# Kernel optimization log

Measured on AMD Instinct MI355X. Metric: run time of the kernel, lower is better.

Reference implementation:

```python
import jax, jax.numpy as jnp
import numpy as np

N = 100000   # num nodes
E = 1200000  # num edges
D = 64       # feature dim (input and both hidden layers)
R = 4        # num relations


def setup_inputs() -> dict:
    key = jax.random.key(0)
    ks = jax.random.split(key, 16)

    def p(k, shape, scale=0.05):
        return jax.random.normal(k, shape, dtype=jnp.float32) * scale

    inp = {
        "x": p(ks[0], (N, D), 1.0),
        "src": jax.random.randint(ks[1], (E,), 0, N),
        "dst": jax.random.randint(ks[2], (E,), 0, N),
        "rel": jax.random.randint(ks[3], (E,), 0, R),
    }
    i = 4
    for layer in (1, 2):
        inp[f"conv{layer}_w"] = p(ks[i], (D, R * D)); i += 1
        inp[f"conv{layer}_b"] = jnp.zeros((D,), jnp.float32)
        inp[f"conv{layer}_ws"] = p(ks[i], (D, D)); i += 1
        inp[f"conv{layer}_bs"] = jnp.zeros((D,), jnp.float32)
        inp[f"hw{layer}_pw"] = p(ks[i], (D, 2 * D)); i += 1
        inp[f"hw{layer}_pb"] = jnp.zeros((D,), jnp.float32)
        inp[f"hw{layer}_tw"] = p(ks[i], (D, 2 * D)); i += 1
        inp[f"hw{layer}_tb"] = jnp.full((D,), -2.0, jnp.float32)  # transform bias init -2
    return inp


def _rgc(x, src, dst, rel, w, b, ws, bs):
    # RelationalGraphConv: per-(node, relation) scatter-mean of source features,
    # then linear over concatenated relation slots + self-loop linear + sigmoid.
    msg = x[src]                                  # [E, D] gather
    seg = dst * R + rel                           # [E] flattened (node, relation) id
    s = jax.ops.segment_sum(msg, seg, num_segments=N * R)          # [N*R, D]
    cnt = jax.ops.segment_sum(jnp.ones((msg.shape[0], 1), msg.dtype), seg,
                              num_segments=N * R)                  # [N*R, 1]
    upd = (s / jnp.maximum(cnt, 1.0)).reshape(N, R * x.shape[1])   # [N, R*D]
    out = upd @ w.T + b + x @ ws.T + bs
    return jax.nn.sigmoid(out)


def _highway(h, prev, pw, pb, tw, tb):
    c = jnp.concatenate([h, prev], axis=1)        # [N, 2D]
    pr = jax.nn.relu(c @ pw.T + pb)
    g = jax.nn.sigmoid(c @ tw.T + tb)
    return g * pr + (1.0 - g) * h


def reference(x, src, dst, rel,
              conv1_w, conv1_b, conv1_ws, conv1_bs,
              hw1_pw, hw1_pb, hw1_tw, hw1_tb,
              conv2_w, conv2_b, conv2_ws, conv2_bs,
              hw2_pw, hw2_pb, hw2_tw, hw2_tb):
    h1 = _rgc(x, src, dst, rel, conv1_w, conv1_b, conv1_ws, conv1_bs)
    g1 = _highway(h1, x, hw1_pw, hw1_pb, hw1_tw, hw1_tb)   # prev_gcn = input
    h2 = _rgc(g1, src, dst, rel, conv2_w, conv2_b, conv2_ws, conv2_bs)
    g2 = _highway(h2, h1, hw2_pw, hw2_pb, hw2_tw, hw2_tb)  # prev_gcn = h1 (conv1 output)
    return g2  # node_feature, [N, D]
```

## Files before the change

### kernel.cpp

```cpp
#include <hip/hip_runtime.h>

#define NN 100000
#define NE 1200000
#define NRR 400000
#define NBIN 392
#define SEGB 1024
#define EPB 4096

typedef float f32x4 __attribute__((ext_vector_type(4)));
typedef __bf16 bf16x8 __attribute__((ext_vector_type(8)));

__device__ __forceinline__ float sigmoidf_(float x){ return 1.0f/(1.0f+__expf(-x)); }

__global__ __launch_bounds__(256)
void binhist_kernel(const int* __restrict__ dst, const int* __restrict__ rel,
                    int* __restrict__ bincnt){
  __shared__ int h[NBIN];
  int t = threadIdx.x;
  for (int i = t; i < NBIN; i += 256) h[i] = 0;
  __syncthreads();
  for (int e = blockIdx.x*256 + t; e < NE; e += 512*256){
    int bin = (dst[e]*4 + rel[e]) >> 10;
    atomicAdd(&h[bin], 1);
  }
  __syncthreads();
  for (int i = t; i < NBIN; i += 256)
    if (h[i]) atomicAdd(&bincnt[i], h[i]);
}

__global__ void binscan_kernel(const int* __restrict__ bincnt, int* __restrict__ binoff,
                               int* __restrict__ bincur, int* __restrict__ soff){
  if (threadIdx.x == 0){
    int s = 0;
    for (int i = 0; i < NBIN; ++i){ binoff[i] = s; bincur[i] = s; s += bincnt[i]; }
    binoff[NBIN] = NE;
    soff[NRR] = NE;
  }
}

__global__ __launch_bounds__(256)
void passA_kernel(const int* __restrict__ src, const int* __restrict__ dst,
                  const int* __restrict__ rel, int* __restrict__ bincur,
                  unsigned* __restrict__ ebin){
  __shared__ int h[NBIN], runbase[NBIN];
  int t = threadIdx.x;
  for (int i = t; i < NBIN; i += 256) h[i] = 0;
  __syncthreads();
  int lo = blockIdx.x*EPB, hi = min(lo + EPB, NE);
  for (int e = lo + t; e < hi; e += 256)
    atomicAdd(&h[(dst[e]*4 + rel[e]) >> 10], 1);
  __syncthreads();
  for (int i = t; i < NBIN; i += 256){
    runbase[i] = h[i] ? atomicAdd(&bincur[i], h[i]) : 0;
    h[i] = 0;
  }
  __syncthreads();
  for (int e = lo + t; e < hi; e += 256){
    int seg = dst[e]*4 + rel[e];
    int bin = seg >> 10;
    int p = runbase[bin] + atomicAdd(&h[bin], 1);
    ebin[p] = (unsigned)src[e] | ((unsigned)(seg & 1023) << 17);
  }
}

__global__ __launch_bounds__(1024)
void passB_kernel(const unsigned* __restrict__ ebin, const int* __restrict__ binoff,
                  int* __restrict__ soff, unsigned* __restrict__ ebuck){
  __shared__ int st[SEGB];
  __shared__ int wsum[16], wbase[16];
  const int bin = blockIdx.x;
  const int t = threadIdx.x;
  const int base = binoff[bin], end = binoff[bin+1];
  st[t] = 0;
  __syncthreads();
  for (int e = base + t; e < end; e += 1024)
    atomicAdd(&st[(ebin[e] >> 17) & 1023], 1);
  __syncthreads();
  int h0 = st[t];
  int lane = t & 63, wv = t >> 6;
  int inc = h0;
  #pragma unroll
  for (int o = 1; o < 64; o <<= 1){ int u = __shfl_up(inc, o); if (lane >= o) inc += u; }
  if (lane == 63) wsum[wv] = inc;
  __syncthreads();
  if (t == 0){ int s = 0; for (int i = 0; i < 16; ++i){ wbase[i] = s; s += wsum[i]; } }
  __syncthreads();
  int ex = base + wbase[wv] + (inc - h0);
  st[t] = ex;
  int sg = bin*SEGB + t;
  if (sg < NRR) soff[sg] = ex;
  __syncthreads();
  for (int e = base + t; e < end; e += 1024){
    unsigned u = ebin[e];
    int p = atomicAdd(&st[(u >> 17) & 1023], 1);
    ebuck[p] = u & 0x1FFFFu;
  }
}

#define TBB 3125
__global__ __launch_bounds__(256)
void tobf16_prep_kernel(const float* __restrict__ xf, __bf16* __restrict__ xb,
                        const float* __restrict__ w,  const float* __restrict__ b,
                        const float* __restrict__ ws, const float* __restrict__ bs,
                        const float* __restrict__ pw, const float* __restrict__ pb,
                        const float* __restrict__ tw, const float* __restrict__ tb,
                        const float* __restrict__ w2,  const float* __restrict__ b2,
                        const float* __restrict__ ws2, const float* __restrict__ bs2,
                        const float* __restrict__ pw2, const float* __restrict__ pb2,
                        const float* __restrict__ tw2, const float* __restrict__ tb2,
                        __bf16* __restrict__ W1a, __bf16* __restrict__ W2a,
                        float* __restrict__ B1a, float* __restrict__ B2a,
                        __bf16* __restrict__ W1b, __bf16* __restrict__ W2b,
                        float* __restrict__ B1b, float* __restrict__ B2b){
  if (blockIdx.x < TBB) {
    int i = (blockIdx.x*256 + threadIdx.x)*8;
    if (i < NN*64){
      f32x4 a = *(const f32x4*)(xf + i);
      f32x4 c = *(const f32x4*)(xf + i + 4);
      bf16x8 r;
      r[0]=(__bf16)a[0]; r[1]=(__bf16)a[1]; r[2]=(__bf16)a[2]; r[3]=(__bf16)a[3];
      r[4]=(__bf16)c[0]; r[5]=(__bf16)c[1]; r[6]=(__bf16)c[2]; r[7]=(__bf16)c[3];
      *(bf16x8*)(xb + i) = r;
    }
    return;
  }
  int i = (blockIdx.x - TBB)*256 + threadIdx.x;
  if (i < 64*320) {
    int e = i & 7, lane = (i >> 3) & 63, j = (i >> 9) & 3, kbi = i >> 11;
    int n = j*16 + (lane & 15);
    int k = kbi*32 + (lane >> 4)*8 + e;
    float va = (k < 256) ? w[n*256 + k]  : ws[n*64 + (k - 256)];
    float vb = (k < 256) ? w2[n*256 + k] : ws2[n*64 + (k - 256)];
    W1a[i] = (__bf16)va;
    W1b[i] = (__bf16)vb;
  }
  if (i < 128*128) {
    int e = i & 7, lane = (i >> 3) & 63, j = (i >> 9) & 7, kbi = i >> 12;
    int n = j*16 + (lane & 15);
    int k = kbi*32 + (lane >> 4)*8 + e;
    float va = (n < 64) ? pw[n*128 + k]  : tw[(n - 64)*128 + k];
    float vb = (n < 64) ? pw2[n*128 + k] : tw2[(n - 64)*128 + k];
    W2a[i] = (__bf16)va;
    W2b[i] = (__bf16)vb;
  }
  if (i < 64)  { B1a[i] = b[i] + bs[i];  B1b[i] = b2[i] + bs2[i]; }
  if (i < 128) { B2a[i] = (i < 64) ? pb[i] : tb[i-64];
                 B2b[i] = (i < 64) ? pb2[i] : tb2[i-64]; }
}

__global__ __launch_bounds__(256)
void gather_kernel(const unsigned* __restrict__ ebuck, const int* __restrict__ soff,
                   const __bf16* __restrict__ inb, __bf16* __restrict__ segb){
  const int sgg = blockIdx.x*32 + (threadIdx.x >> 3);
  const int fl  = threadIdx.x & 7;
  const int e0 = soff[sgg];
  const int e1 = soff[sgg + 1];
  const int c  = e1 - e0;

  int idx[8];
  #pragma unroll
  for (int k = 0; k < 8; ++k) idx[k] = (int)ebuck[e0 + k];

  f32x4 a0 = {0.f,0.f,0.f,0.f}, a1 = {0.f,0.f,0.f,0.f};
  f32x4 b0 = {0.f,0.f,0.f,0.f}, b1 = {0.f,0.f,0.f,0.f};
  #pragma unroll
  for (int k = 0; k < 8; ++k) {
    if (k < c) {
      bf16x8 v = *(const bf16x8*)(&inb[(size_t)idx[k]*64 + fl*8]);
      if (k & 1) {
        b0[0]+=(float)v[0]; b0[1]+=(float)v[1]; b0[2]+=(float)v[2]; b0[3]+=(float)v[3];
        b1[0]+=(float)v[4]; b1[1]+=(float)v[5]; b1[2]+=(float)v[6]; b1[3]+=(float)v[7];
      } else {
        a0[0]+=(float)v[0]; a0[1]+=(float)v[1]; a0[2]+=(float)v[2]; a0[3]+=(float)v[3];
        a1[0]+=(float)v[4]; a1[1]+=(float)v[5]; a1[2]+=(float)v[6]; a1[3]+=(float)v[7];
      }
    }
  }
  for (int i = 8; i < c; i += 2) {
    int s0 = (int)ebuck[e0 + i];
    bf16x8 v0 = *(const bf16x8*)(&inb[(size_t)s0*64 + fl*8]);
    a0[0]+=(float)v0[0]; a0[1]+=(float)v0[1]; a0[2]+=(float)v0[2]; a0[3]+=(float)v0[3];
    a1[0]+=(float)v0[4]; a1[1]+=(float)v0[5]; a1[2]+=(float)v0[6]; a1[3]+=(float)v0[7];
    if (i + 1 < c) {
      int s1 = (int)ebuck[e0 + i + 1];
      bf16x8 v1 = *(const bf16x8*)(&inb[(size_t)s1*64 + fl*8]);
      b0[0]+=(float)v1[0]; b0[1]+=(float)v1[1]; b0[2]+=(float)v1[2]; b0[3]+=(float)v1[3];
      b1[0]+=(float)v1[4]; b1[1]+=(float)v1[5]; b1[2]+=(float)v1[6]; b1[3]+=(float)v1[7];
    }
  }
  float inv = 1.0f / fmaxf((float)c, 1.0f);
  bf16x8 r;
  r[0]=(__bf16)((a0[0]+b0[0])*inv); r[1]=(__bf16)((a0[1]+b0[1])*inv);
  r[2]=(__bf16)((a0[2]+b0[2])*inv); r[3]=(__bf16)((a0[3]+b0[3])*inv);
  r[4]=(__bf16)((a1[0]+b1[0])*inv); r[5]=(__bf16)((a1[1]+b1[1])*inv);
  r[6]=(__bf16)((a1[2]+b1[2])*inv); r[7]=(__bf16)((a1[3]+b1[3])*inv);

  const int n   = sgg >> 2, rr = sgg & 3;
  const int nb  = n >> 4,  ml = n & 15;
  const int kbi = rr*2 + (fl >> 2);
  const int kgs = fl & 3;
  *(bf16x8*)(&segb[(size_t)((nb*8 + kbi)*64 + kgs*16 + ml)*8]) = r;
}

#define HSP 72

template<bool LAYER1>
__global__ __launch_bounds__(256, 4)
void dense_kernel(const __bf16* __restrict__ segbs,
                  const __bf16* __restrict__ xinb,
                  const __bf16* __restrict__ prevb,
                  const __bf16* __restrict__ W1s,
                  const __bf16* __restrict__ W2s,
                  const float* __restrict__ bias1,
                  const float* __restrict__ bias2,
                  __bf16* __restrict__ hb,
                  __bf16* __restrict__ gb,
                  float* __restrict__ outp)
{
  __shared__ __align__(16) __bf16 hs[64*HSP];
  __shared__ __align__(16) float outs[64*64];

  const int tid  = threadIdx.x;
  const int lane = tid & 63;
  const int wv   = tid >> 6;
  const int mloc = lane & 15;
  const int kg   = lane >> 4;
  const int wb   = blockIdx.x*64 + wv*16;
  const int arow = min(wb + mloc, NN-1);
  const int nbq  = min(wb, NN-16) >> 4;
  const size_t abase = (size_t)nbq * (8*512);

  f32x4 acc1[4] = {};

  #pragma unroll
  for (int kbi = 0; kbi < 8; ++kbi) {
    bf16x8 af = *(const bf16x8*)(&segbs[abase + (size_t)(kbi*64 + lane)*8]);
    #pragma unroll
    for (int j = 0; j < 4; ++j) {
      bf16x8 bf = *(const bf16x8*)(&W1s[((kbi*4 + j)*64 + lane)*8]);
      acc1[j] = __builtin_amdgcn_mfma_f32_16x16x32_bf16(af, bf, acc1[j], 0,0,0);
    }
  }
  #pragma unroll
  for (int kb = 0; kb < 64; kb += 32) {
    bf16x8 af = *(const bf16x8*)(&xinb[(size_t)arow*64 + kb + kg*8]);
    const int kbi = 8 + (kb >> 5);
    #pragma unroll
    for (int j = 0; j < 4; ++j) {
      bf16x8 bf = *(const bf16x8*)(&W1s[((kbi*4 + j)*64 + lane)*8]);
      acc1[j] = __builtin_amdgcn_mfma_f32_16x16x32_bf16(af, bf, acc1[j], 0,0,0);
    }
  }

  #pragma unroll
  for (int j = 0; j < 4; ++j) {
    int col = j*16 + mloc;
    float b1 = bias1[col];
    #pragma unroll
    for (int r = 0; r < 4; ++r) {
      float hv = sigmoidf_(acc1[j][r] + b1);
      acc1[j][r] = hv;
      hs[(wv*16 + kg*4 + r)*HSP + col] = (__bf16)hv;
    }
  }

  if (LAYER1) {
    #pragma unroll
    for (int i = 0; i < 2; ++i) {
      int r2 = i*8 + (lane >> 3);
      int c2 = lane & 7;
      bf16x8 v = *(const bf16x8*)(&hs[(wv*16 + r2)*HSP + c2*8]);
      int grow = wb + r2;
      if (grow < NN) *(bf16x8*)(&hb[(size_t)grow*64 + c2*8]) = v;
    }
  }

  f32x4 acc2[8] = {};
  #pragma unroll
  for (int kb = 0; kb < 64; kb += 32) {
    bf16x8 af = *(const bf16x8*)(&hs[(wv*16 + mloc)*HSP + kb + kg*8]);
    const int kbi = kb >> 5;
    #pragma unroll
    for (int j = 0; j < 8; ++j) {
      bf16x8 bf = *(const bf16x8*)(&W2s[((kbi*8 + j)*64 + lane)*8]);
      acc2[j] = __builtin_amdgcn_mfma_f32_16x16x32_bf16(af, bf, acc2[j], 0,0,0);
    }
  }
  #pragma unroll
  for (int kb = 0; kb < 64; kb += 32) {
    bf16x8 af = *(const bf16x8*)(&prevb[(size_t)arow*64 + kb + kg*8]);
    const int kbi = 2 + (kb >> 5);
    #pragma unroll
    for (int j = 0; j < 8; ++j) {
      bf16x8 bf = *(const bf16x8*)(&W2s[((kbi*8 + j)*64 + lane)*8]);
      acc2[j] = __builtin_amdgcn_mfma_f32_16x16x32_bf16(af, bf, acc2[j], 0,0,0);
    }
  }

  #pragma unroll
  for (int j = 0; j < 4; ++j) {
    int col = j*16 + mloc;
    float bp = bias2[col];
    float bt = bias2[64 + col];
    #pragma unroll
    for (int r = 0; r < 4; ++r) {
      float pr = fmaxf(acc2[j][r] + bp, 0.0f);
      float g  = sigmoidf_(acc2[j+4][r] + bt);
      float hv = acc1[j][r];
      float ov = g*pr + (1.0f - g)*hv;
      if (LAYER1) {
        hs[(wv*16 + kg*4 + r)*HSP + col] = (__bf16)ov;
      } else {
        outs[(wv*16 + kg*4 + r)*64 + col] = ov;
      }
    }
  }
  if (LAYER1) {
    #pragma unroll
    for (int i = 0; i < 2; ++i) {
      int r2 = i*8 + (lane >> 3);
      int c2 = lane & 7;
      bf16x8 v = *(const bf16x8*)(&hs[(wv*16 + r2)*HSP + c2*8]);
      int grow = wb + r2;
      if (grow < NN) *(bf16x8*)(&gb[(size_t)grow*64 + c2*8]) = v;
    }
  } else {
    #pragma unroll
    for (int i = 0; i < 4; ++i) {
      int pos = i*256 + lane*4;
      int r2 = pos >> 6, c2 = pos & 63;
      int grow = wb + r2;
      if (grow < NN)
        *(f32x4*)(&outp[(size_t)grow*64 + c2]) =
            *(const f32x4*)(&outs[(wv*16 + r2)*64 + c2]);
    }
  }
}

extern "C" void kernel_launch(void* const* d_in, const int* in_sizes, int n_in,
                              void* d_out, int out_size, void* d_ws, size_t ws_size,
                              hipStream_t stream){
  const float* x    = (const float*)d_in[0];
  const int*   src  = (const int*)d_in[1];
  const int*   dst  = (const int*)d_in[2];
  const int*   rel  = (const int*)d_in[3];
  const float* c1w  = (const float*)d_in[4];
  const float* c1b  = (const float*)d_in[5];
  const float* c1ws = (const float*)d_in[6];
  const float* c1bs = (const float*)d_in[7];
  const float* h1pw = (const float*)d_in[8];
  const float* h1pb = (const float*)d_in[9];
  const float* h1tw = (const float*)d_in[10];
  const float* h1tb = (const float*)d_in[11];
  const float* c2w  = (const float*)d_in[12];
  const float* c2b  = (const float*)d_in[13];
  const float* c2ws = (const float*)d_in[14];
  const float* c2bs = (const float*)d_in[15];
  const float* h2pw = (const float*)d_in[16];
  const float* h2pb = (const float*)d_in[17];
  const float* h2tw = (const float*)d_in[18];
  const float* h2tb = (const float*)d_in[19];

  char* p = (char*)d_ws;
  __bf16* segb = (__bf16*)p;  p += (size_t)NRR*64*2;
  __bf16* xb   = (__bf16*)p;  p += (size_t)NN*64*2;
  __bf16* h1b  = (__bf16*)p;  p += (size_t)NN*64*2;
  __bf16* g1b  = (__bf16*)p;  p += (size_t)NN*64*2;
  unsigned* ebuck = (unsigned*)p; p += (size_t)(NE+16)*4;
  unsigned* ebin  = (unsigned*)p; p += (size_t)NE*4;
  int* soff    = (int*)p;     p += (size_t)(NRR+8)*4;
  int* bincnt  = (int*)p;     p += 512*4;
  int* binoff  = (int*)p;     p += 512*4;
  int* bincur  = (int*)p;     p += 512*4;
  __bf16* W1a  = (__bf16*)p;  p += 64*320*2;
  __bf16* W2a  = (__bf16*)p;  p += 128*128*2;
  __bf16* W1b  = (__bf16*)p;  p += 64*320*2;
  __bf16* W2b  = (__bf16*)p;  p += 128*128*2;
  float* B1a   = (float*)p;   p += 64*4;
  float* B2a   = (float*)p;   p += 128*4;
  float* B1b   = (float*)p;   p += 64*4;
  float* B2b   = (float*)p;   p += 128*4;

  float* out = (float*)d_out;

  hipMemsetAsync(bincnt, 0, 512*4, stream);
  binhist_kernel<<<512, 256, 0, stream>>>(dst, rel, bincnt);
  binscan_kernel<<<1, 64, 0, stream>>>(bincnt, binoff, bincur, soff);
  passA_kernel<<<(NE+EPB-1)/EPB, 256, 0, stream>>>(src, dst, rel, bincur, ebin);
  passB_kernel<<<NBIN, 1024, 0, stream>>>(ebin, binoff, soff, ebuck);

  tobf16_prep_kernel<<<TBB+80, 256, 0, stream>>>(x, xb,
                                      c1w, c1b, c1ws, c1bs, h1pw, h1pb, h1tw, h1tb,
                                      c2w, c2b, c2ws, c2bs, h2pw, h2pb, h2tw, h2tb,
                                      W1a, W2a, B1a, B2a, W1b, W2b, B1b, B2b);

  gather_kernel<<<NRR/32, 256, 0, stream>>>(ebuck, soff, xb, segb);
  dense_kernel<true><<<(NN+63)/64, 256, 0, stream>>>(segb, xb, xb, W1a, W2a, B1a, B2a,
                                                     h1b, g1b, nullptr);
  gather_kernel<<<NRR/32, 256, 0, stream>>>(ebuck, soff, g1b, segb);
  dense_kernel<false><<<(NN+63)/64, 256, 0, stream>>>(segb, g1b, h1b, W1b, W2b, B1b, B2b,
                                                      nullptr, nullptr, out);
}
```

Before: 300.4 us.

## Fuse scatter-mean gather into dense layer kernel via shared-memory tiles

Merges the per-(node,relation) gather/mean kernel into the dense MFMA kernel. Each block gathers its 64 nodes' 256 segments straight into an LDS tile laid out in MFMA operand order, along with the self-feature rows, then runs both matmuls from LDS. This removes the bf16 segb intermediate (global write and reread) and two launches per forward. In exchange each block does more serial gather work (8 segments per thread group), occupancy drops to 3 blocks, and the gather loses the dual-accumulator unroll for high-degree segments.

```diff
diff --git a/kernel.cpp b/kernel.cpp
--- a/kernel.cpp
+++ b/kernel.cpp
@@ -148,66 +148,12 @@
                  B2b[i] = (i < 64) ? pb2[i] : tb2[i-64]; }
 }
 
-__global__ __launch_bounds__(256)
-void gather_kernel(const unsigned* __restrict__ ebuck, const int* __restrict__ soff,
-                   const __bf16* __restrict__ inb, __bf16* __restrict__ segb){
-  const int sgg = blockIdx.x*32 + (threadIdx.x >> 3);
-  const int fl  = threadIdx.x & 7;
-  const int e0 = soff[sgg];
-  const int e1 = soff[sgg + 1];
-  const int c  = e1 - e0;
-
-  int idx[8];
-  #pragma unroll
-  for (int k = 0; k < 8; ++k) idx[k] = (int)ebuck[e0 + k];
-
-  f32x4 a0 = {0.f,0.f,0.f,0.f}, a1 = {0.f,0.f,0.f,0.f};
-  f32x4 b0 = {0.f,0.f,0.f,0.f}, b1 = {0.f,0.f,0.f,0.f};
-  #pragma unroll
-  for (int k = 0; k < 8; ++k) {
-    if (k < c) {
-      bf16x8 v = *(const bf16x8*)(&inb[(size_t)idx[k]*64 + fl*8]);
-      if (k & 1) {
-        b0[0]+=(float)v[0]; b0[1]+=(float)v[1]; b0[2]+=(float)v[2]; b0[3]+=(float)v[3];
-        b1[0]+=(float)v[4]; b1[1]+=(float)v[5]; b1[2]+=(float)v[6]; b1[3]+=(float)v[7];
-      } else {
-        a0[0]+=(float)v[0]; a0[1]+=(float)v[1]; a0[2]+=(float)v[2]; a0[3]+=(float)v[3];
-        a1[0]+=(float)v[4]; a1[1]+=(float)v[5]; a1[2]+=(float)v[6]; a1[3]+=(float)v[7];
-      }
-    }
-  }
-  for (int i = 8; i < c; i += 2) {
-    int s0 = (int)ebuck[e0 + i];
-    bf16x8 v0 = *(const bf16x8*)(&inb[(size_t)s0*64 + fl*8]);
-    a0[0]+=(float)v0[0]; a0[1]+=(float)v0[1]; a0[2]+=(float)v0[2]; a0[3]+=(float)v0[3];
-    a1[0]+=(float)v0[4]; a1[1]+=(float)v0[5]; a1[2]+=(float)v0[6]; a1[3]+=(float)v0[7];
-    if (i + 1 < c) {
-      int s1 = (int)ebuck[e0 + i + 1];
-      bf16x8 v1 = *(const bf16x8*)(&inb[(size_t)s1*64 + fl*8]);
-      b0[0]+=(float)v1[0]; b0[1]+=(float)v1[1]; b0[2]+=(float)v1[2]; b0[3]+=(float)v1[3];
-      b1[0]+=(float)v1[4]; b1[1]+=(float)v1[5]; b1[2]+=(float)v1[6]; b1[3]+=(float)v1[7];
-    }
-  }
-  float inv = 1.0f / fmaxf((float)c, 1.0f);
-  bf16x8 r;
-  r[0]=(__bf16)((a0[0]+b0[0])*inv); r[1]=(__bf16)((a0[1]+b0[1])*inv);
-  r[2]=(__bf16)((a0[2]+b0[2])*inv); r[3]=(__bf16)((a0[3]+b0[3])*inv);
-  r[4]=(__bf16)((a1[0]+b1[0])*inv); r[5]=(__bf16)((a1[1]+b1[1])*inv);
-  r[6]=(__bf16)((a1[2]+b1[2])*inv); r[7]=(__bf16)((a1[3]+b1[3])*inv);
-
-  const int n   = sgg >> 2, rr = sgg & 3;
-  const int nb  = n >> 4,  ml = n & 15;
-  const int kbi = rr*2 + (fl >> 2);
-  const int kgs = fl & 3;
-  *(bf16x8*)(&segb[(size_t)((nb*8 + kbi)*64 + kgs*16 + ml)*8]) = r;
-}
-
-#define HSP 72
+#define ASW (10*64*8)
 
 template<bool LAYER1>
-__global__ __launch_bounds__(256, 4)
-void dense_kernel(const __bf16* __restrict__ segbs,
-                  const __bf16* __restrict__ xinb,
+__global__ __launch_bounds__(256, 3)
+void fused_kernel(const unsigned* __restrict__ ebuck, const int* __restrict__ soff,
+                  const __bf16* __restrict__ inb,
                   const __bf16* __restrict__ prevb,
                   const __bf16* __restrict__ W1s,
                   const __bf16* __restrict__ W2s,
@@ -217,40 +163,89 @@
                   __bf16* __restrict__ gb,
                   float* __restrict__ outp)
 {
-  __shared__ __align__(16) __bf16 hs[64*HSP];
-  __shared__ __align__(16) float outs[64*64];
+  __shared__ __align__(16) __bf16 As[4*ASW];
 
   const int tid  = threadIdx.x;
   const int lane = tid & 63;
   const int wv   = tid >> 6;
+  const int g    = tid >> 3;
+  const int fl   = tid & 7;
+  const int base = blockIdx.x*64;
+  const int wb   = base + wv*16;
+
+  for (int si = 0; si < 8; ++si) {
+    const int sw  = g*8 + si;
+    const int sgg = blockIdx.x*256 + sw;
+    const int e0 = soff[min(sgg, NRR)];
+    const int e1 = soff[min(sgg + 1, NRR)];
+    const int c  = e1 - e0;
+
+    int idx[8];
+    #pragma unroll
+    for (int k = 0; k < 8; ++k) idx[k] = (int)ebuck[e0 + k];
+
+    f32x4 a0 = {0.f,0.f,0.f,0.f}, a1 = {0.f,0.f,0.f,0.f};
+    f32x4 b0 = {0.f,0.f,0.f,0.f}, b1 = {0.f,0.f,0.f,0.f};
+    #pragma unroll
+    for (int k = 0; k < 8; ++k) {
+      if (k < c) {
+        bf16x8 v = *(const bf16x8*)(&inb[(size_t)idx[k]*64 + fl*8]);
+        if (k & 1) {
+          b0[0]+=(float)v[0]; b0[1]+=(float)v[1]; b0[2]+=(float)v[2]; b0[3]+=(float)v[3];
+          b1[0]+=(float)v[4]; b1[1]+=(float)v[5]; b1[2]+=(float)v[6]; b1[3]+=(float)v[7];
+        } else {
+          a0[0]+=(float)v[0]; a0[1]+=(float)v[1]; a0[2]+=(float)v[2]; a0[3]+=(float)v[3];
+          a1[0]+=(float)v[4]; a1[1]+=(float)v[5]; a1[2]+=(float)v[6]; a1[3]+=(float)v[7];
+        }
+      }
+    }
+    for (int i = 8; i < c; ++i) {
+      int s0 = (int)ebuck[e0 + i];
+      bf16x8 v0 = *(const bf16x8*)(&inb[(size_t)s0*64 + fl*8]);
+      a0[0]+=(float)v0[0]; a0[1]+=(float)v0[1]; a0[2]+=(float)v0[2]; a0[3]+=(float)v0[3];
+      a1[0]+=(float)v0[4]; a1[1]+=(float)v0[5]; a1[2]+=(float)v0[6]; a1[3]+=(float)v0[7];
+    }
+    float inv = 1.0f / fmaxf((float)c, 1.0f);
+    bf16x8 r;
+    r[0]=(__bf16)((a0[0]+b0[0])*inv); r[1]=(__bf16)((a0[1]+b0[1])*inv);
+    r[2]=(__bf16)((a0[2]+b0[2])*inv); r[3]=(__bf16)((a0[3]+b0[3])*inv);
+    r[4]=(__bf16)((a1[0]+b1[0])*inv); r[5]=(__bf16)((a1[1]+b1[1])*inv);
+    r[6]=(__bf16)((a1[2]+b1[2])*inv); r[7]=(__bf16)((a1[3]+b1[3])*inv);
+
+    const int ml  = (sw >> 2) & 15;
+    const int rr  = sw & 3;
+    const int kbi = rr*2 + (fl >> 2);
+    const int kgs = fl & 3;
+    *(bf16x8*)(&As[(size_t)wv*ASW + ((kbi*64) + kgs*16 + ml)*8]) = r;
+  }
+
+  #pragma unroll
+  for (int it = 0; it < 2; ++it) {
+    int idx = it*64 + lane;
+    int r2w = idx >> 3, oc = idx & 7;
+    int grow = min(wb + r2w, NN-1);
+    bf16x8 v = *(const bf16x8*)(&inb[(size_t)grow*64 + oc*8]);
+    int kbi = 8 + (oc >> 2);
+    int kg2 = oc & 3;
+    *(bf16x8*)(&As[(size_t)wv*ASW + ((kbi*64) + kg2*16 + r2w)*8]) = v;
+  }
+
+  __syncthreads();
+
   const int mloc = lane & 15;
   const int kg   = lane >> 4;
-  const int wb   = blockIdx.x*64 + wv*16;
   const int arow = min(wb + mloc, NN-1);
-  const int nbq  = min(wb, NN-16) >> 4;
-  const size_t abase = (size_t)nbq * (8*512);
 
   f32x4 acc1[4] = {};
-
-  #pragma unroll
-  for (int kbi = 0; kbi < 8; ++kbi) {
-    bf16x8 af = *(const bf16x8*)(&segbs[abase + (size_t)(kbi*64 + lane)*8]);
+  #pragma unroll
+  for (int kbi = 0; kbi < 10; ++kbi) {
+    bf16x8 af = *(const bf16x8*)(&As[(size_t)wv*ASW + (kbi*64 + lane)*8]);
     #pragma unroll
     for (int j = 0; j < 4; ++j) {
       bf16x8 bf = *(const bf16x8*)(&W1s[((kbi*4 + j)*64 + lane)*8]);
       acc1[j] = __builtin_amdgcn_mfma_f32_16x16x32_bf16(af, bf, acc1[j], 0,0,0);
     }
   }
-  #pragma unroll
-  for (int kb = 0; kb < 64; kb += 32) {
-    bf16x8 af = *(const bf16x8*)(&xinb[(size_t)arow*64 + kb + kg*8]);
-    const int kbi = 8 + (kb >> 5);
-    #pragma unroll
-    for (int j = 0; j < 4; ++j) {
-      bf16x8 bf = *(const bf16x8*)(&W1s[((kbi*4 + j)*64 + lane)*8]);
-      acc1[j] = __builtin_amdgcn_mfma_f32_16x16x32_bf16(af, bf, acc1[j], 0,0,0);
-    }
-  }
 
   #pragma unroll
   for (int j = 0; j < 4; ++j) {
@@ -260,7 +255,8 @@
     for (int r = 0; r < 4; ++r) {
       float hv = sigmoidf_(acc1[j][r] + b1);
       acc1[j][r] = hv;
-      hs[(wv*16 + kg*4 + r)*HSP + col] = (__bf16)hv;
+      int row = kg*4 + r;
+      As[(size_t)wv*ASW + (((col>>5)*64) + ((col>>3)&3)*16 + row)*8 + (col&7)] = (__bf16)hv;
     }
   }
 
@@ -269,7 +265,7 @@
     for (int i = 0; i < 2; ++i) {
       int r2 = i*8 + (lane >> 3);
       int c2 = lane & 7;
-      bf16x8 v = *(const bf16x8*)(&hs[(wv*16 + r2)*HSP + c2*8]);
+      bf16x8 v = *(const bf16x8*)(&As[(size_t)wv*ASW + (((c2>>2)*64) + (c2&3)*16 + r2)*8]);
       int grow = wb + r2;
       if (grow < NN) *(bf16x8*)(&hb[(size_t)grow*64 + c2*8]) = v;
     }
@@ -277,9 +273,8 @@
 
   f32x4 acc2[8] = {};
   #pragma unroll
-  for (int kb = 0; kb < 64; kb += 32) {
-    bf16x8 af = *(const bf16x8*)(&hs[(wv*16 + mloc)*HSP + kb + kg*8]);
-    const int kbi = kb >> 5;
+  for (int kbi = 0; kbi < 2; ++kbi) {
+    bf16x8 af = *(const bf16x8*)(&As[(size_t)wv*ASW + (kbi*64 + lane)*8]);
     #pragma unroll
     for (int j = 0; j < 8; ++j) {
       bf16x8 bf = *(const bf16x8*)(&W2s[((kbi*8 + j)*64 + lane)*8]);
@@ -287,12 +282,13 @@
     }
   }
   #pragma unroll
-  for (int kb = 0; kb < 64; kb += 32) {
-    bf16x8 af = *(const bf16x8*)(&prevb[(size_t)arow*64 + kb + kg*8]);
-    const int kbi = 2 + (kb >> 5);
+  for (int kk = 0; kk < 2; ++kk) {
+    bf16x8 af;
+    if (LAYER1) af = *(const bf16x8*)(&As[(size_t)wv*ASW + ((8+kk)*64 + lane)*8]);
+    else        af = *(const bf16x8*)(&prevb[(size_t)arow*64 + kk*32 + kg*8]);
     #pragma unroll
     for (int j = 0; j < 8; ++j) {
-      bf16x8 bf = *(const bf16x8*)(&W2s[((kbi*8 + j)*64 + lane)*8]);
+      bf16x8 bf = *(const bf16x8*)(&W2s[(((2+kk)*8 + j)*64 + lane)*8]);
       acc2[j] = __builtin_amdgcn_mfma_f32_16x16x32_bf16(af, bf, acc2[j], 0,0,0);
     }
   }
@@ -305,13 +301,15 @@
     #pragma unroll
     for (int r = 0; r < 4; ++r) {
       float pr = fmaxf(acc2[j][r] + bp, 0.0f);
-      float g  = sigmoidf_(acc2[j+4][r] + bt);
+      float gg = sigmoidf_(acc2[j+4][r] + bt);
       float hv = acc1[j][r];
-      float ov = g*pr + (1.0f - g)*hv;
+      float ov = gg*pr + (1.0f - gg)*hv;
+      int row = kg*4 + r;
       if (LAYER1) {
-        hs[(wv*16 + kg*4 + r)*HSP + col] = (__bf16)ov;
+        As[(size_t)wv*ASW + (((col>>5)*64) + ((col>>3)&3)*16 + row)*8 + (col&7)] = (__bf16)ov;
       } else {
-        outs[(wv*16 + kg*4 + r)*64 + col] = ov;
+        float* outs_w = (float*)((char*)As + (size_t)wv*ASW*2);
+        outs_w[row*64 + col] = ov;
       }
     }
   }
@@ -320,11 +318,12 @@
     for (int i = 0; i < 2; ++i) {
       int r2 = i*8 + (lane >> 3);
       int c2 = lane & 7;
-      bf16x8 v = *(const bf16x8*)(&hs[(wv*16 + r2)*HSP + c2*8]);
+      bf16x8 v = *(const bf16x8*)(&As[(size_t)wv*ASW + (((c2>>2)*64) + (c2&3)*16 + r2)*8]);
       int grow = wb + r2;
       if (grow < NN) *(bf16x8*)(&gb[(size_t)grow*64 + c2*8]) = v;
     }
   } else {
+    const float* outs_w = (const float*)((const char*)As + (size_t)wv*ASW*2);
     #pragma unroll
     for (int i = 0; i < 4; ++i) {
       int pos = i*256 + lane*4;
@@ -332,7 +331,7 @@
       int grow = wb + r2;
       if (grow < NN)
         *(f32x4*)(&outp[(size_t)grow*64 + c2]) =
-            *(const f32x4*)(&outs[(wv*16 + r2)*64 + c2]);
+            *(const f32x4*)(&outs_w[r2*64 + c2]);
     }
   }
 }
@@ -362,7 +361,6 @@
   const float* h2tb = (const float*)d_in[19];
 
   char* p = (char*)d_ws;
-  __bf16* segb = (__bf16*)p;  p += (size_t)NRR*64*2;
   __bf16* xb   = (__bf16*)p;  p += (size_t)NN*64*2;
   __bf16* h1b  = (__bf16*)p;  p += (size_t)NN*64*2;
   __bf16* g1b  = (__bf16*)p;  p += (size_t)NN*64*2;
@@ -394,10 +392,10 @@
                                       c2w, c2b, c2ws, c2bs, h2pw, h2pb, h2tw, h2tb,
                                       W1a, W2a, B1a, B2a, W1b, W2b, B1b, B2b);
 
-  gather_kernel<<<NRR/32, 256, 0, stream>>>(ebuck, soff, xb, segb);
-  dense_kernel<true><<<(NN+63)/64, 256, 0, stream>>>(segb, xb, xb, W1a, W2a, B1a, B2a,
+  fused_kernel<true><<<(NN+63)/64, 256, 0, stream>>>(ebuck, soff, xb, xb,
+                                                     W1a, W2a, B1a, B2a,
                                                      h1b, g1b, nullptr);
-  gather_kernel<<<NRR/32, 256, 0, stream>>>(ebuck, soff, g1b, segb);
-  dense_kernel<false><<<(NN+63)/64, 256, 0, stream>>>(segb, g1b, h1b, W1b, W2b, B1b, B2b,
+  fused_kernel<false><<<(NN+63)/64, 256, 0, stream>>>(ebuck, soff, g1b, h1b,
+                                                      W1b, W2b, B1b, B2b,
                                                       nullptr, nullptr, out);
 }
```

Result: slower. 339.1 us (+12.9%).
